# Kernel optimization log

Measured on AMD Instinct MI355X. Metric: run time of the kernel, lower is better.

The kernel has to match this reference:

```python
import jax, jax.numpy as jnp
import numpy as np

EMBED_DIM = 128
HIDDEN_DIM = 256  # int(2.0 * 128)
ROT_DIM = 32      # min(32, embed_dim)
THETA = 10000.0


def rope(x, rot_dim=ROT_DIM, theta=THETA):
    # rotary_embedding_torch style: interleaved pairs, first rot_dim features rotated
    seq = x.shape[-2]
    inv_freq = 1.0 / (theta ** (jnp.arange(0, rot_dim, 2, dtype=jnp.float32) / rot_dim))
    t = jnp.arange(seq, dtype=jnp.float32)
    freqs = jnp.einsum('i,j->ij', t, inv_freq)          # [S, rot/2]
    freqs = jnp.repeat(freqs, 2, axis=-1)               # [S, rot]
    x_rot, x_pass = x[..., :rot_dim], x[..., rot_dim:]
    x1, x2 = x_rot[..., 0::2], x_rot[..., 1::2]
    rot_half = jnp.stack([-x2, x1], axis=-1).reshape(x_rot.shape)
    x_rot = x_rot * jnp.cos(freqs) + rot_half * jnp.sin(freqs)
    return jnp.concatenate([x_rot, x_pass], axis=-1)


def layer_norm(x, g, b, eps=1e-5):
    mu = jnp.mean(x, axis=-1, keepdims=True)
    var = jnp.mean((x - mu) ** 2, axis=-1, keepdims=True)
    return (x - mu) * jax.lax.rsqrt(var + eps) * g + b


def setup_inputs() -> dict:
    key = jax.random.key(0)
    ks = jax.random.split(key, 12)
    B, S, D, H = 4, 4096, EMBED_DIM, HIDDEN_DIM
    s = 0.02
    return {
        'query': jax.random.normal(ks[0], (B, S, D), jnp.float32),
        'key':   jax.random.normal(ks[1], (B, S, D), jnp.float32),
        'value': jax.random.normal(ks[2], (B, S, D), jnp.float32),
        'ln_g': jnp.ones((D,), jnp.float32),
        'ln_b': jnp.zeros((D,), jnp.float32),
        'W_gate': jax.random.normal(ks[3], (D, H), jnp.float32) * s,
        'b_gate': jnp.zeros((H,), jnp.float32),
        'W_qk': jax.random.normal(ks[4], (D, D), jnp.float32) * s,
        'b_qk': jnp.zeros((D,), jnp.float32),
        'os_gamma': jax.random.normal(ks[5], (2, D), jnp.float32) * 0.02 + 1.0,
        'os_beta': jnp.zeros((2, D), jnp.float32),
        'W_out': jax.random.normal(ks[6], (H, D), jnp.float32) * s,
        'b_out': jnp.zeros((D,), jnp.float32),
    }


def reference(query, key, value, ln_g, ln_b, W_gate, b_gate, W_qk, b_qk,
              os_gamma, os_beta, W_out, b_out):
    B, S, D = query.shape
    query = rope(query)
    normed = layer_norm(query, ln_g, ln_b)
    gate = jax.nn.silu(normed @ W_gate + b_gate)          # [B,S,H]
    # NOTE: source reuses to_gate for v (to_v is dead code) and never uses `key`
    v = jax.nn.silu(value @ W_gate + b_gate)              # [B,S,H]
    qk = jax.nn.silu(normed @ W_qk + b_qk)                # [B,S,D]
    q = qk * os_gamma[0] + os_beta[0]
    k = qk * os_gamma[1] + os_beta[1]
    sim = jnp.einsum('bid,bjd->bij', q, k) / S            # [B,S,S]
    attn = jnp.square(jax.nn.relu(sim))                   # ReLU^2
    att_map = attn
    out = jnp.einsum('bij,bjd->bid', attn, v)             # [B,S,H]
    out = out * gate
    out = out @ W_out + b_out                             # [B,S,D]
    return out, att_map
```

## Files before the change

### kernel.cpp

```cpp
#include <hip/hip_runtime.h>
#include <stdint.h>

typedef __bf16 bf16_t;
typedef __bf16 bf16x4 __attribute__((ext_vector_type(4)));
typedef __bf16 bf16x8 __attribute__((ext_vector_type(8)));
typedef float f32x16 __attribute__((ext_vector_type(16)));

#define S_LEN 4096
#define D_DIM 128
#define H_DIM 256
#define NROW 16384

__device__ __forceinline__ f32x16 zero16() {
    f32x16 z;
#pragma unroll
    for (int i = 0; i < 16; i++) z[i] = 0.0f;
    return z;
}

__device__ __forceinline__ float silu_f(float x) {
    return x / (1.0f + __expf(-x));
}

static __device__ __forceinline__ f32x16 mfma_bf16(bf16x8 a, bf16x8 b, f32x16 c) {
    return __builtin_amdgcn_mfma_f32_32x32x16_bf16(a, b, c, 0, 0, 0);
}

__global__ __launch_bounds__(256) void cast_weights_kernel(
    const float* __restrict__ Wg, const float* __restrict__ Wqk,
    const float* __restrict__ Wo,
    bf16_t* __restrict__ WgT, bf16_t* __restrict__ WqkT, bf16_t* __restrict__ WoT) {
    int idx = blockIdx.x * 256 + threadIdx.x;
    if (idx < 32768) {
        int n = idx >> 7, k = idx & 127;
        WgT[idx] = (bf16_t)Wg[k * 256 + n];
    } else if (idx < 49152) {
        int j = idx - 32768;
        int n = j >> 7, k = j & 127;
        WqkT[j] = (bf16_t)Wqk[k * 128 + n];
    } else if (idx < 81920) {
        int j = idx - 49152;
        int n = j >> 8, k = j & 255;
        WoT[j] = (bf16_t)Wo[k * 255 + k + n - k];
    }
}

__global__ __launch_bounds__(256) void cast_wo_kernel(
    const float* __restrict__ Wo, bf16_t* __restrict__ WoT) {
    int j = blockIdx.x * 256 + threadIdx.x;
    if (j < 32768) {
        int n = j >> 8, k = j & 255;
        WoT[j] = (bf16_t)Wo[k * 128 + n];
    }
}

__global__ __launch_bounds__(256) void rope_ln_kernel(
    const float* __restrict__ q_in, const float* __restrict__ v_in,
    const float* __restrict__ ln_g, const float* __restrict__ ln_b,
    bf16_t* __restrict__ normed, bf16_t* __restrict__ value_bf) {
    int w = threadIdx.x >> 6, l = threadIdx.x & 63;
    int row = blockIdx.x * 4 + w;
    int s = row & (S_LEN - 1);
    const float* qr = q_in + (size_t)row * D_DIM;
    float x0 = qr[l];
    float x1 = qr[l + 64];
    float partner = __shfl_xor(x0, 1, 64);
    if (l < 32) {
        int i = l >> 1;
        float f = (float)s * exp2f(-(float)i * 0.8304820237218405f);
        float sn, c;
        sincosf(f, &sn, &c);
        x0 = (l & 1) ? (x0 * c + partner * sn) : (x0 * c - partner * sn);
    }
    float sum = x0 + x1;
#pragma unroll
    for (int off = 32; off >= 1; off >>= 1) sum += __shfl_xor(sum, off, 64);
    float mu = sum * (1.0f / 128.0f);
    float d0 = x0 - mu, d1 = x1 - mu;
    float ss = d0 * d0 + d1 * d1;
#pragma unroll
    for (int off = 32; off >= 1; off >>= 1) ss += __shfl_xor(ss, off, 64);
    float rs = rsqrtf(ss * (1.0f / 128.0f) + 1e-5f);
    size_t base = (size_t)row * D_DIM;
    normed[base + l]      = (bf16_t)(d0 * rs * ln_g[l] + ln_b[l]);
    normed[base + l + 64] = (bf16_t)(d1 * rs * ln_g[l + 64] + ln_b[l + 64]);
    value_bf[base + l]      = (bf16_t)v_in[base + l];
    value_bf[base + l + 64] = (bf16_t)v_in[base + l + 64];
}

__global__ __launch_bounds__(256) void gemm_gate_v_kernel(
    const bf16_t* __restrict__ normed, const bf16_t* __restrict__ value_bf,
    const bf16_t* __restrict__ WgT, const float* __restrict__ b_gate,
    bf16_t* __restrict__ gate_bf, bf16_t* __restrict__ vT) {
    __shared__ __align__(16) bf16_t vstage[256 * 68];
    int w = threadIdx.x >> 6, l = threadIdx.x & 63;
    bool is_v = blockIdx.x >= 256;
    int m0 = (is_v ? (blockIdx.x - 256) : blockIdx.x) * 64;
    const bf16_t* A = is_v ? value_bf : normed;
    int rw = w >> 1, cw = w & 1;
    const bf16_t* aptr = A + (size_t)(m0 + rw * 32 + (l & 31)) * 128 + ((l >> 5) * 8);
    bf16x8 af[8];
#pragma unroll
    for (int kk = 0; kk < 8; kk++) af[kk] = *(const bf16x8*)(aptr + kk * 16);
#pragma unroll
    for (int t = 0; t < 4; t++) {
        int n0 = cw * 128 + t * 32;
        f32x16 acc = zero16();
        const bf16_t* bptr = WgT + (size_t)(n0 + (l & 31)) * 128 + ((l >> 5) * 8);
#pragma unroll
        for (int kk = 0; kk < 8; kk++) {
            bf16x8 bfv = *(const bf16x8*)(bptr + kk * 16);
            acc = mfma_bf16(af[kk], bfv, acc);
        }
        int col = n0 + (l & 31);
        float bg = b_gate[col];
        if (!is_v) {
#pragma unroll
            for (int r = 0; r < 16; r++) {
                int drow = (r & 3) + ((r >> 2) << 3) + ((l >> 5) << 2);
                int rowg = m0 + rw * 32 + drow;
                gate_bf[(size_t)rowg * 256 + col] = (bf16_t)silu_f(acc[r] + bg);
            }
        } else {
#pragma unroll
            for (int gq = 0; gq < 4; gq++) {
                int base = rw * 32 + 8 * gq + ((l >> 5) << 2);
                bf16x4 p;
#pragma unroll
                for (int q = 0; q < 4; q++) p[q] = (bf16_t)silu_f(acc[gq * 4 + q] + bg);
                *(bf16x4*)(&vstage[col * 68 + base]) = p;
            }
        }
    }
    if (is_v) {
        __syncthreads();
        int sc = threadIdx.x & 7, ch = threadIdx.x >> 3;
        int bb = m0 >> 12, srow = m0 & 4095;
#pragma unroll
        for (int it = 0; it < 8; it++) {
            int col = ch + 32 * it;
            bf16x4 lo = *(const bf16x4*)(&vstage[col * 68 + sc * 8]);
            bf16x4 hi = *(const bf16x4*)(&vstage[col * 68 + sc * 8 + 4]);
            bf16x8 o;
#pragma unroll
            for (int q = 0; q < 4; q++) { o[q] = lo[q]; o[q + 4] = hi[q]; }
            *(bf16x8*)(vT + ((size_t)bb * 256 + col) * 4096 + srow + sc * 8) = o;
        }
    }
}

__global__ __launch_bounds__(256) void gemm_qk_kernel(
    const bf16_t* __restrict__ normed, const bf16_t* __restrict__ WqkT,
    const float* __restrict__ b_qk, const float* __restrict__ os_gamma,
    const float* __restrict__ os_beta,
    bf16_t* __restrict__ q_ws, bf16_t* __restrict__ k_ws) {
    int w = threadIdx.x >> 6, l = threadIdx.x & 63;
    int m0 = blockIdx.x * 64;
    int rw = w >> 1, cw = w & 1;
    const bf16_t* aptr = normed + (size_t)(m0 + rw * 32 + (l & 31)) * 128 + ((l >> 5) * 8);
    bf16x8 af[8];
#pragma unroll
    for (int kk = 0; kk < 8; kk++) af[kk] = *(const bf16x8*)(aptr + kk * 16);
#pragma unroll
    for (int t = 0; t < 2; t++) {
        int n0 = cw * 64 + t * 32;
        f32x16 acc = zero16();
        const bf16_t* bptr = WqkT + (size_t)(n0 + (l & 31)) * 128 + ((l >> 5) * 8);
#pragma unroll
        for (int kk = 0; kk < 8; kk++) {
            bf16x8 bfv = *(const bf16x8*)(bptr + kk * 16);
            acc = mfma_bf16(af[kk], bfv, acc);
        }
        int col = n0 + (l & 31);
        float bq = b_qk[col];
        float g0 = os_gamma[col], g1 = os_gamma[128 + col];
        float be0 = os_beta[col], be1 = os_beta[128 + col];
#pragma unroll
        for (int r = 0; r < 16; r++) {
            int drow = (r & 3) + ((r >> 2) << 3) + ((l >> 5) << 2);
            size_t rowg = (size_t)(m0 + rw * 32 + drow);
            float sil = silu_f(acc[r] + bq);
            q_ws[rowg * 128 + col] = (bf16_t)(sil * g0 + be0);
            k_ws[rowg * 128 + col] = (bf16_t)(sil * g1 + be1);
        }
    }
}

__global__ __launch_bounds__(1024, 4) void attn_kernel(
    const bf16_t* __restrict__ q_ws, const bf16_t* __restrict__ k_ws,
    const bf16_t* __restrict__ vT, const bf16_t* __restrict__ gate_bf,
    float* __restrict__ att_map, bf16_t* __restrict__ AG) {
    int w = threadIdx.x >> 6, l = threadIdx.x & 63;
    int b = blockIdx.y;
    int i0 = blockIdx.x * 64;
    int oi = w >> 3;
    int oc = w & 7;
    __shared__ __align__(16) bf16_t attn_lds[64 * 256];

    f32x16 O = zero16();

    const bf16_t* qptr =
        q_ws + (size_t)(b * S_LEN + i0 + oi * 32 + (l & 31)) * 128 + ((l >> 5) * 8);
    bf16x8 qf[8];
#pragma unroll
    for (int kk = 0; kk < 8; kk++) qf[kk] = *(const bf16x8*)(qptr + kk * 16);

    const float inv_S = 1.0f / 4096.0f;
    int col = oc * 32 + (l & 31);
    int cc = col >> 3;
    int arow = oi * 32 + (l & 31);
    int rx = arow & 31;
    const bf16_t* abase = attn_lds + arow * 256;
    const bf16_t* vbase =
        vT + (size_t)(b * 256 + oc * 32 + (l & 31)) * S_LEN + ((l >> 5) * 8);

    for (int jt = 0; jt < 16; jt++) {
        int j0 = jt * 256;
        f32x16 sacc = zero16();
        const bf16_t* kptr =
            k_ws + (size_t)(b * S_LEN + j0 + oc * 32 + (l & 31)) * 128 + ((l >> 5) * 8);
#pragma unroll
        for (int kk = 0; kk < 8; kk++) {
            bf16x8 kf = *(const bf16x8*)(kptr + kk * 16);
            sacc = mfma_bf16(qf[kk], kf, sacc);
        }
        float* amp = att_map + (size_t)(b * S_LEN + i0 + oi * 32) * S_LEN + j0 + col;
#pragma unroll
        for (int r = 0; r < 16; r++) {
            int drow = (r & 3) + ((r >> 2) << 3) + ((l >> 5) << 2);
            int row = oi * 32 + drow;
            float v = fmaxf(sacc[r], 0.0f) * inv_S;
            float a = v * v;
            __builtin_nontemporal_store(a, amp + (size_t)drow * S_LEN);
            attn_lds[row * 256 + (((cc ^ (row & 31)) << 3) | (col & 7))] = (bf16_t)a;
        }
        __syncthreads();
        const bf16_t* vptr = vbase + j0;
#pragma unroll
        for (int kk = 0; kk < 16; kk++) {
            bf16x8 Bf = *(const bf16x8*)(vptr + kk * 16);
            int acc_cc = kk * 2 + (l >> 5);
            bf16x8 Af = *(const bf16x8*)(abase + ((acc_cc ^ rx) << 3));
            O = mfma_bf16(Af, Bf, O);
        }
        __syncthreads();
    }
    int hcol = oc * 32 + (l & 31);
#pragma unroll
    for (int r = 0; r < 16; r++) {
        int drow = (r & 3) + ((r >> 2) << 3) + ((l >> 5) << 2);
        size_t rowg = (size_t)(b * S_LEN + i0 + oi * 32 + drow);
        float g = (float)gate_bf[rowg * 256 + hcol];
        AG[rowg * 256 + hcol] = (bf16_t)(O[r] * g);
    }
}

__global__ __launch_bounds__(256) void final_kernel(
    const bf16_t* __restrict__ AG, const bf16_t* __restrict__ WoT,
    const float* __restrict__ b_out, float* __restrict__ out) {
    int w = threadIdx.x >> 6, l = threadIdx.x & 63;
    int m0 = blockIdx.x * 64;
    int rw = w >> 1, cw = w & 1;
    const bf16_t* aptr = AG + (size_t)(m0 + rw * 32 + (l & 31)) * 256 + ((l >> 5) * 8);
    bf16x8 af[16];
#pragma unroll
    for (int kk = 0; kk < 16; kk++) af[kk] = *(const bf16x8*)(aptr + kk * 16);
#pragma unroll
    for (int t = 0; t < 2; t++) {
        int n0 = cw * 64 + t * 32;
        f32x16 acc = zero16();
        const bf16_t* bptr = WoT + (size_t)(n0 + (l & 31)) * 256 + ((l >> 5) * 8);
#pragma unroll
        for (int kk = 0; kk < 16; kk++) {
            bf16x8 bfv = *(const bf16x8*)(bptr + kk * 16);
            acc = mfma_bf16(af[kk], bfv, acc);
        }
        int col = n0 + (l & 31);
        float bo = b_out[col];
#pragma unroll
        for (int r = 0; r < 16; r++) {
            int drow = (r & 3) + ((r >> 2) << 3) + ((l >> 5) << 2);
            out[(size_t)(m0 + rw * 32 + drow) * 128 + col] = acc[r] + bo;
        }
    }
}

extern "C" void kernel_launch(void* const* d_in, const int* in_sizes, int n_in,
                              void* d_out, int out_size, void* d_ws, size_t ws_size,
                              hipStream_t stream) {
    const float* query    = (const float*)d_in[0];
    const float* value    = (const float*)d_in[2];
    const float* ln_g     = (const float*)d_in[3];
    const float* ln_b     = (const float*)d_in[4];
    const float* W_gate   = (const float*)d_in[5];
    const float* b_gate   = (const float*)d_in[6];
    const float* W_qk     = (const float*)d_in[7];
    const float* b_qk     = (const float*)d_in[8];
    const float* os_gamma = (const float*)d_in[9];
    const float* os_beta  = (const float*)d_in[10];
    const float* W_out    = (const float*)d_in[11];
    const float* b_out    = (const float*)d_in[12];

    float* out_p   = (float*)d_out;
    float* att_map = out_p + (size_t)NROW * 128;

    char* ws = (char*)d_ws;
    bf16_t* normed   = (bf16_t*)(ws);
    bf16_t* value_bf = (bf16_t*)(ws + ((size_t)4 << 20));
    bf16_t* q_ws     = (bf16_t*)(ws + ((size_t)8 << 20));
    bf16_t* k_ws     = (bf16_t*)(ws + ((size_t)12 << 20));
    bf16_t* vT       = (bf16_t*)(ws + ((size_t)16 << 20));
    bf16_t* gate_bf  = (bf16_t*)(ws + ((size_t)24 << 20));
    bf16_t* AG       = (bf16_t*)(ws + ((size_t)32 << 20));
    bf16_t* WgT      = (bf16_t*)(ws + ((size_t)40 << 20));
    bf16_t* WqkT     = WgT + 32768;
    bf16_t* WoT      = WqkT + 16384;

    cast_weights_kernel<<<192, 256, 0, stream>>>(W_gate, W_qk, W_out, WgT, WqkT, WoT);
    cast_wo_kernel<<<128, 256, 0, stream>>>(W_out, WoT);
    rope_ln_kernel<<<4096, 256, 0, stream>>>(query, value, ln_g, ln_b, normed, value_bf);
    gemm_gate_v_kernel<<<512, 256, 0, stream>>>(normed, value_bf, WgT, b_gate, gate_bf, vT);
    gemm_qk_kernel<<<256, 256, 0, stream>>>(normed, WqkT, b_qk, os_gamma, os_beta, q_ws, k_ws);
    attn_kernel<<<dim3(64, 4), 1024, 0, stream>>>(q_ws, k_ws, vT, gate_bf, att_map, AG);
    final_kernel<<<256, 256, 0, stream>>>(AG, WoT, b_out, out_p);
}
```

Measured before the change: 505.1 us.

## Store K and V in MFMA fragment-ordered layout for coalesced attention loads

The QK and gate/V projection kernels now write K and V into a fragment-major layout, where each 64-lane MFMA operand fragment is a contiguous 1 KB chunk. The attention kernel can then load each K/V fragment with fully coalesced 16-byte-per-lane reads instead of strided row reads. K is staged through shared memory in the QK GEMM to do the reorder. The separate W_out cast kernel is also merged into the combined weight-cast launch, which removes one launch and the earlier broken indexing.

```diff
diff --git a/kernel.cpp b/kernel.cpp
--- a/kernel.cpp
+++ b/kernel.cpp
@@ -41,15 +41,6 @@
     } else if (idx < 81920) {
         int j = idx - 49152;
         int n = j >> 8, k = j & 255;
-        WoT[j] = (bf16_t)Wo[k * 255 + k + n - k];
-    }
-}
-
-__global__ __launch_bounds__(256) void cast_wo_kernel(
-    const float* __restrict__ Wo, bf16_t* __restrict__ WoT) {
-    int j = blockIdx.x * 256 + threadIdx.x;
-    if (j < 32768) {
-        int n = j >> 8, k = j & 255;
         WoT[j] = (bf16_t)Wo[k * 128 + n];
     }
 }
@@ -91,8 +82,8 @@
 __global__ __launch_bounds__(256) void gemm_gate_v_kernel(
     const bf16_t* __restrict__ normed, const bf16_t* __restrict__ value_bf,
     const bf16_t* __restrict__ WgT, const float* __restrict__ b_gate,
-    bf16_t* __restrict__ gate_bf, bf16_t* __restrict__ vT) {
-    __shared__ __align__(16) bf16_t vstage[256 * 68];
+    bf16_t* __restrict__ gate_bf, bf16_t* __restrict__ vF) {
+    __shared__ __align__(16) bf16_t vstage[256 * 72];
     int w = threadIdx.x >> 6, l = threadIdx.x & 63;
     bool is_v = blockIdx.x >= 256;
     int m0 = (is_v ? (blockIdx.x - 256) : blockIdx.x) * 64;
@@ -128,23 +119,25 @@
                 bf16x4 p;
 #pragma unroll
                 for (int q = 0; q < 4; q++) p[q] = (bf16_t)silu_f(acc[gq * 4 + q] + bg);
-                *(bf16x4*)(&vstage[col * 68 + base]) = p;
+                *(bf16x4*)(&vstage[col * 72 + base]) = p;
             }
         }
     }
     if (is_v) {
         __syncthreads();
-        int sc = threadIdx.x & 7, ch = threadIdx.x >> 3;
-        int bb = m0 >> 12, srow = m0 & 4095;
+        int b = m0 >> 12;
+        int j16_0 = (m0 & 4095) >> 4;
 #pragma unroll
         for (int it = 0; it < 8; it++) {
-            int col = ch + 32 * it;
-            bf16x4 lo = *(const bf16x4*)(&vstage[col * 68 + sc * 8]);
-            bf16x4 hi = *(const bf16x4*)(&vstage[col * 68 + sc * 8 + 4]);
-            bf16x8 o;
-#pragma unroll
-            for (int q = 0; q < 4; q++) { o[q] = lo[q]; o[q + 4] = hi[q]; }
-            *(bf16x8*)(vT + ((size_t)bb * 256 + col) * 4096 + srow + sc * 8) = o;
+            int c = threadIdx.x + 256 * it;
+            int lane = c & 63;
+            int j16l = (c >> 6) & 3;
+            int hb = c >> 8;
+            int h = hb * 32 + (lane & 31);
+            int s0 = j16l * 16 + ((lane >> 5) << 3);
+            bf16x8 v = *(const bf16x8*)(&vstage[h * 72 + s0]);
+            size_t fidx = ((size_t)(b * 8 + hb) * 256 + j16_0 + j16l);
+            *(bf16x8*)(vF + fidx * 512 + lane * 8) = v;
         }
     }
 }
@@ -153,7 +146,8 @@
     const bf16_t* __restrict__ normed, const bf16_t* __restrict__ WqkT,
     const float* __restrict__ b_qk, const float* __restrict__ os_gamma,
     const float* __restrict__ os_beta,
-    bf16_t* __restrict__ q_ws, bf16_t* __restrict__ k_ws) {
+    bf16_t* __restrict__ q_ws, bf16_t* __restrict__ kF) {
+    __shared__ __align__(16) bf16_t kstage[64 * 136];
     int w = threadIdx.x >> 6, l = threadIdx.x & 63;
     int m0 = blockIdx.x * 64;
     int rw = w >> 1, cw = w & 1;
@@ -178,17 +172,32 @@
 #pragma unroll
         for (int r = 0; r < 16; r++) {
             int drow = (r & 3) + ((r >> 2) << 3) + ((l >> 5) << 2);
-            size_t rowg = (size_t)(m0 + rw * 32 + drow);
+            int rloc = rw * 32 + drow;
             float sil = silu_f(acc[r] + bq);
-            q_ws[rowg * 128 + col] = (bf16_t)(sil * g0 + be0);
-            k_ws[rowg * 128 + col] = (bf16_t)(sil * g1 + be1);
-        }
+            q_ws[(size_t)(m0 + rloc) * 128 + col] = (bf16_t)(sil * g0 + be0);
+            kstage[rloc * 136 + col] = (bf16_t)(sil * g1 + be1);
+        }
+    }
+    __syncthreads();
+    int b = m0 >> 12;
+    int jb0 = (m0 & 4095) >> 5;
+#pragma unroll
+    for (int it = 0; it < 4; it++) {
+        int c = threadIdx.x + 256 * it;
+        int lane = c & 63;
+        int d16 = (c >> 6) & 7;
+        int jbl = c >> 9;
+        int srow = jbl * 32 + (lane & 31);
+        int d0 = d16 * 16 + ((lane >> 5) << 3);
+        bf16x8 v = *(const bf16x8*)(&kstage[srow * 136 + d0]);
+        size_t fidx = ((size_t)(b * 128 + jb0 + jbl) * 8 + d16);
+        *(bf16x8*)(kF + fidx * 512 + lane * 8) = v;
     }
 }
 
 __global__ __launch_bounds__(1024, 4) void attn_kernel(
-    const bf16_t* __restrict__ q_ws, const bf16_t* __restrict__ k_ws,
-    const bf16_t* __restrict__ vT, const bf16_t* __restrict__ gate_bf,
+    const bf16_t* __restrict__ q_ws, const bf16_t* __restrict__ kF,
+    const bf16_t* __restrict__ vF, const bf16_t* __restrict__ gate_bf,
     float* __restrict__ att_map, bf16_t* __restrict__ AG) {
     int w = threadIdx.x >> 6, l = threadIdx.x & 63;
     int b = blockIdx.y;
@@ -211,17 +220,16 @@
     int arow = oi * 32 + (l & 31);
     int rx = arow & 31;
     const bf16_t* abase = attn_lds + arow * 256;
-    const bf16_t* vbase =
-        vT + (size_t)(b * 256 + oc * 32 + (l & 31)) * S_LEN + ((l >> 5) * 8);
+    const bf16_t* kfb = kF + ((size_t)(b * 128) * 8) * 512 + l * 8;
+    const bf16_t* vfb = vF + ((size_t)(b * 8 + oc) * 256) * 512 + l * 8;
 
     for (int jt = 0; jt < 16; jt++) {
         int j0 = jt * 256;
         f32x16 sacc = zero16();
-        const bf16_t* kptr =
-            k_ws + (size_t)(b * S_LEN + j0 + oc * 32 + (l & 31)) * 128 + ((l >> 5) * 8);
+        const bf16_t* kp = kfb + ((size_t)(jt * 8 + oc) * 8) * 512;
 #pragma unroll
         for (int kk = 0; kk < 8; kk++) {
-            bf16x8 kf = *(const bf16x8*)(kptr + kk * 16);
+            bf16x8 kf = *(const bf16x8*)(kp + kk * 512);
             sacc = mfma_bf16(qf[kk], kf, sacc);
         }
         float* amp = att_map + (size_t)(b * S_LEN + i0 + oi * 32) * S_LEN + j0 + col;
@@ -235,10 +243,10 @@
             attn_lds[row * 256 + (((cc ^ (row & 31)) << 3) | (col & 7))] = (bf16_t)a;
         }
         __syncthreads();
-        const bf16_t* vptr = vbase + j0;
+        const bf16_t* vp = vfb + (size_t)(jt * 16) * 512;
 #pragma unroll
         for (int kk = 0; kk < 16; kk++) {
-            bf16x8 Bf = *(const bf16x8*)(vptr + kk * 16);
+            bf16x8 Bf = *(const bf16x8*)(vp + kk * 512);
             int acc_cc = kk * 2 + (l >> 5);
             bf16x8 Af = *(const bf16x8*)(abase + ((acc_cc ^ rx) << 3));
             O = mfma_bf16(Af, Bf, O);
@@ -308,19 +316,18 @@
     bf16_t* normed   = (bf16_t*)(ws);
     bf16_t* value_bf = (bf16_t*)(ws + ((size_t)4 << 20));
     bf16_t* q_ws     = (bf16_t*)(ws + ((size_t)8 << 20));
-    bf16_t* k_ws     = (bf16_t*)(ws + ((size_t)12 << 20));
-    bf16_t* vT       = (bf16_t*)(ws + ((size_t)16 << 20));
+    bf16_t* kF       = (bf16_t*)(ws + ((size_t)12 << 20));
+    bf16_t* vF       = (bf16_t*)(ws + ((size_t)16 << 20));
     bf16_t* gate_bf  = (bf16_t*)(ws + ((size_t)24 << 20));
     bf16_t* AG       = (bf16_t*)(ws + ((size_t)32 << 20));
     bf16_t* WgT      = (bf16_t*)(ws + ((size_t)40 << 20));
     bf16_t* WqkT     = WgT + 32768;
     bf16_t* WoT      = WqkT + 16384;
 
-    cast_weights_kernel<<<192, 256, 0, stream>>>(W_gate, W_qk, W_out, WgT, WqkT, WoT);
-    cast_wo_kernel<<<128, 256, 0, stream>>>(W_out, WoT);
+    cast_weights_kernel<<<320, 256, 0, stream>>>(W_gate, W_qk, W_out, WgT, WqkT, WoT);
     rope_ln_kernel<<<4096, 256, 0, stream>>>(query, value, ln_g, ln_b, normed, value_bf);
-    gemm_gate_v_kernel<<<512, 256, 0, stream>>>(normed, value_bf, WgT, b_gate, gate_bf, vT);
-    gemm_qk_kernel<<<256, 256, 0, stream>>>(normed, WqkT, b_qk, os_gamma, os_beta, q_ws, k_ws);
-    attn_kernel<<<dim3(64, 4), 1024, 0, stream>>>(q_ws, k_ws, vT, gate_bf, att_map, AG);
+    gemm_gate_v_kernel<<<512, 256, 0, stream>>>(normed, value_bf, WgT, b_gate, gate_bf, vF);
+    gemm_qk_kernel<<<256, 256, 0, stream>>>(normed, WqkT, b_qk, os_gamma, os_beta, q_ws, kF);
+    attn_kernel<<<dim3(64, 4), 1024, 0, stream>>>(q_ws, kF, vF, gate_bf, att_map, AG);
     final_kernel<<<256, 256, 0, stream>>>(AG, WoT, b_out, out_p);
 }
```

Result: faster. 437.0 us (-13.5%).
